# Optimization experiments

Hardware: AMD Instinct MI355X
Metric: run time of the kernel (lower is better)

## Reference

```python
import jax, jax.numpy as jnp
import numpy as np

DECAY = 0.99
EPSILON = 1e-05


def setup_inputs() -> dict:
    key = jax.random.key(0)
    k1, k2, k3, k4 = jax.random.split(key, 4)
    B, S, D, K = 16, 2048, 512, 2048
    x = jax.random.normal(k1, (B, S, D), dtype=jnp.float32)
    embed = jax.random.normal(k2, (K, D), dtype=jnp.float32)
    cluster_size = jax.random.uniform(k3, (K,), dtype=jnp.float32)
    embed_avg = jax.random.normal(k4, (K, D), dtype=jnp.float32)
    return {"x": x, "embed": embed, "cluster_size": cluster_size, "embed_avg": embed_avg}


def reference(x, embed, cluster_size, embed_avg):
    # x: [B,S,D]  embed: [K,D]  cluster_size: [K]  embed_avg: [K,D]
    B, S, D = x.shape
    K = embed.shape[0]
    xf = x.reshape(-1, D)  # [N,D], N=B*S

    # quantize(): negative squared euclidean distance, argmax over codebook
    x_sq = jnp.sum(xf * xf, axis=1, keepdims=True)            # [N,1]
    e_sq = jnp.sum(embed * embed, axis=1)[None, :]            # [1,K]
    dist = -(x_sq - 2.0 * (xf @ embed.T) + e_sq)              # [N,K]
    embed_ind = jnp.argmax(dist, axis=-1)                     # [N] int

    # dequantize
    quantize = embed[embed_ind].reshape(B, S, D)

    # training EMA updates (onehot.sum(0) and x^T @ onehot expressed as segment sums)
    ones = jnp.ones((xf.shape[0],), dtype=x.dtype)
    bins = jax.ops.segment_sum(ones, embed_ind, num_segments=K)        # [K] == onehot.sum(0)
    embed_sum_t = jax.ops.segment_sum(xf, embed_ind, num_segments=K)   # [K,D] == (x.T @ onehot).T

    new_cluster_size = cluster_size * DECAY + (1.0 - DECAY) * bins
    new_embed_avg = embed_avg * DECAY + (1.0 - DECAY) * embed_sum_t

    total = new_cluster_size.sum()
    smoothed = (new_cluster_size + EPSILON) / (total + K * EPSILON) * total  # laplace smoothing
    new_embed = new_embed_avg / smoothed[:, None]

    return (quantize,
            embed_ind.reshape(B, S),
            dist.reshape(B, S, K),
            new_cluster_size,
            new_embed_avg,
            new_embed)
```

## Files before the change

### kernel.cpp

```cpp
#include <hip/hip_runtime.h>

#define DECAY 0.99f
#define OMD   0.01f
#define EPS   1e-5f

constexpr int Bb = 16, Ss = 2048, Dd = 512, Kk = 2048;
constexpr int Nn = Bb * Ss;
constexpr int RP = 1088;

typedef __attribute__((ext_vector_type(8))) short short8;
typedef __attribute__((ext_vector_type(4))) float f32x4;

__device__ __forceinline__ unsigned short f2bf(float x) {
    unsigned u = __float_as_uint(x);
    unsigned r = (u + 0x7FFFu + ((u >> 16) & 1u)) >> 16;
    return (unsigned short)r;
}
__device__ __forceinline__ float bf2f(unsigned short u) {
    return __uint_as_float((unsigned)u << 16);
}

__device__ __forceinline__ void gload_lds16(const void* g, void* l) {
    __builtin_amdgcn_global_load_lds(
        (const __attribute__((address_space(1))) void*)g,
        (__attribute__((address_space(3))) void*)l, 16, 0, 0);
}

__device__ __forceinline__ short8 swap16(short8 v) {
    union { short8 s; unsigned u[4]; } a, b;
    a.s = v;
    #pragma unroll
    for (int i = 0; i < 4; ++i) b.u[i] = (a.u[i] >> 16) | (a.u[i] << 16);
    return b.s;
}

#define BARRIER() do { asm volatile("" ::: "memory"); \
                       __builtin_amdgcn_s_barrier();  \
                       asm volatile("" ::: "memory"); } while (0)

__global__ void rows_sq(const float* __restrict__ in, float* __restrict__ out, int nrows) {
    int row  = blockIdx.x * 4 + (threadIdx.x >> 6);
    int lane = threadIdx.x & 63;
    if (row >= nrows) return;
    const float4* p = (const float4*)(in + (size_t)row * Dd);
    float s = 0.f;
    #pragma unroll
    for (int i = 0; i < 2; ++i) {
        float4 v = p[lane + 64 * i];
        s += v.x * v.x + v.y * v.y + v.z * v.z + v.w * v.w;
    }
    #pragma unroll
    for (int off = 32; off; off >>= 1) s += __shfl_down(s, off);
    if (lane == 0) out[row] = s;
}

__global__ void conv_ilv(const float* __restrict__ in,
                         unsigned short* __restrict__ out,
                         float* __restrict__ sq) {
    int row  = blockIdx.x * 4 + (threadIdx.x >> 6);
    int lane = threadIdx.x & 63;
    const float4* p = (const float4*)(in + (size_t)row * Dd);
    uint4* o = (uint4*)(out + (size_t)row * RP);
    float s = 0.f;
    #pragma unroll
    for (int i = 0; i < 2; ++i) {
        int idx = lane + 64 * i;
        float4 v = p[idx];
        float f[4] = {v.x, v.y, v.z, v.w};
        unsigned d[4];
        #pragma unroll
        for (int j = 0; j < 4; ++j) {
            float x = f[j];
            s += x * x;
            unsigned short h = f2bf(x);
            unsigned short m = f2bf(x - bf2f(h));
            d[j] = ((unsigned)m << 16) | h;
        }
        o[idx] = make_uint4(d[0], d[1], d[2], d[3]);
    }
    #pragma unroll
    for (int off = 32; off; off >>= 1) s += __shfl_down(s, off);
    if (lane == 0) sq[row] = s;
}

__global__ __launch_bounds__(512, 1) void gemm_ilv(
    const unsigned short* __restrict__ xhm,
    const unsigned short* __restrict__ ehm,
    const float* __restrict__ xsq,
    const float* __restrict__ esq,
    float* __restrict__ dist,
    unsigned long long* __restrict__ packed)
{
    __shared__ unsigned short As[2][256][64];
    __shared__ unsigned short Bs[2][256][64];

    const int tid  = threadIdx.x;
    const int lane = tid & 63;
    const int wid  = tid >> 6;
    const int wr   = wid >> 2;
    const int wc   = wid & 3;

    int bid = blockIdx.x;
    int wg  = (bid & 7) * 128 + (bid >> 3);
    int mb  = wg >> 3, nb = wg & 7;
    const int row0 = mb * 256, col0 = nb * 256;

    f32x4 acc[8][4] = {};

    const int l8   = lane >> 3;
    const int csrc = (lane & 7) ^ l8;

    auto stageT = [&](const unsigned short* pl, unsigned short (*dst)[64],
                      int base, int t) {
        #pragma unroll
        for (int jj = 0; jj < 4; ++jj) {
            int rowbase = jj * 64 + wid * 8;
            int row = rowbase + l8;
            const unsigned short* src =
                pl + (size_t)(base + row) * RP + t * 64 + csrc * 8;
            gload_lds16(src, &dst[rowbase][0]);
        }
    };

    auto readA = [&](int d, int g, short8* out) {
        #pragma unroll
        for (int m = 0; m < 8; ++m) {
            int r = wr * 128 + m * 16 + (lane & 15);
            int c = (g * 4 + (lane >> 4)) ^ (r & 7);
            out[m] = *(const short8*)&As[d][r][c * 8];
        }
    };
    auto readB = [&](int d, int g, short8* out) {
        #pragma unroll
        for (int n = 0; n < 4; ++n) {
            int r = wc * 64 + n * 16 + (lane & 15);
            int c = (g * 4 + (lane >> 4)) ^ (r & 7);
            out[n] = *(const short8*)&Bs[d][r][c * 8];
        }
    };

    stageT(xhm, As[0], row0, 0);
    stageT(ehm, Bs[0], col0, 0);
    asm volatile("s_waitcnt vmcnt(0)" ::: "memory");
    BARRIER();

    for (int t = 0; t < 16; ++t) {
        const int cur = t & 1, nxt = cur ^ 1;
        if (t < 15) {
            stageT(xhm, As[nxt], row0, t + 1);
            stageT(ehm, Bs[nxt], col0, t + 1);
        }

        #pragma unroll
        for (int g = 0; g < 2; ++g) {
            short8 va[8], vb[4], vb2[4];
            readA(cur, g, va);
            readB(cur, g, vb);
            #pragma unroll
            for (int n = 0; n < 4; ++n) vb2[n] = swap16(vb[n]);
            #pragma unroll
            for (int m = 0; m < 8; ++m)
                #pragma unroll
                for (int n = 0; n < 4; ++n)
                    acc[m][n] = __builtin_amdgcn_mfma_f32_16x16x32_bf16(
                        va[m], vb[n], acc[m][n], 0, 0, 0);
            #pragma unroll
            for (int m = 0; m < 8; ++m)
                #pragma unroll
                for (int n = 0; n < 4; ++n)
                    acc[m][n] = __builtin_amdgcn_mfma_f32_16x16x32_bf16(
                        va[m], vb2[n], acc[m][n], 0, 0, 0);
        }

        asm volatile("s_waitcnt vmcnt(0)" ::: "memory");
        BARRIER();
    }

    const int jrow = (lane >> 4) * 4;
    const int ncol = lane & 15;
    #pragma unroll
    for (int m = 0; m < 8; ++m) {
        int rbase = row0 + wr * 128 + m * 16 + jrow;
        #pragma unroll
        for (int j = 0; j < 4; ++j) {
            int row = rbase + j;
            float xs = xsq[row];
            float best = -3.4e38f; int bi = 0;
            #pragma unroll
            for (int n = 0; n < 4; ++n) {
                int col = col0 + wc * 64 + n * 16 + ncol;
                float v = 2.f * acc[m][n][j] - xs - esq[col];
                dist[(size_t)row * Kk + col] = v;
                if (v > best) { best = v; bi = col; }
            }
            unsigned u = __float_as_uint(best);
            u = (u & 0x80000000u) ? ~u : (u | 0x80000000u);
            unsigned long long pk = ((unsigned long long)u << 32) | (unsigned)(~bi);
            #pragma unroll
            for (int off = 1; off < 16; off <<= 1) {
                unsigned long long o = __shfl_xor(pk, off);
                if (o > pk) pk = o;
            }
            if (ncol == 0) atomicMax(&packed[row], pk);
        }
    }
}

__global__ void gather_scatter_packed(const float* __restrict__ x,
                                      const float* __restrict__ embed,
                                      const unsigned long long* __restrict__ packed,
                                      float* __restrict__ quant,
                                      float* __restrict__ ind_f,
                                      float* __restrict__ esum,
                                      int* __restrict__ bins) {
    int n = blockIdx.x;
    int k = (int)(~(unsigned)(packed[n] & 0xFFFFFFFFull));
    int t = threadIdx.x;
    size_t xb = (size_t)n * Dd;
    size_t eb = (size_t)k * Dd;
    float v0 = x[xb + t];
    float v1 = x[xb + t + 256];
    quant[xb + t]       = embed[eb + t];
    quant[xb + t + 256] = embed[eb + t + 256];
    atomicAdd(&esum[eb + t],       v0);
    atomicAdd(&esum[eb + t + 256], v1);
    if (t == 0) { ind_f[n] = (float)k; atomicAdd(&bins[k], 1); }
}

#define BM 64
#define BN 64
#define BK 32
__global__ __launch_bounds__(256) void gemm_dist(
    const float* __restrict__ A, const float* __restrict__ Bm_,
    const float* __restrict__ xsq, const float* __restrict__ esq,
    float* __restrict__ dist)
{
    __shared__ float Asl[BK][BM + 4];
    __shared__ float Bsl[BK][BN + 4];
    int tid = threadIdx.x;
    int row0 = blockIdx.x * BM, col0 = blockIdx.y * BN;
    int tx = tid & 15, ty = tid >> 4;
    float acc[4][4] = {};
    int lr = tid >> 3, lc = (tid & 7) * 4;
    for (int d0 = 0; d0 < Dd; d0 += BK) {
        float4 a0 = *(const float4*)(A   + (size_t)(row0 + lr)      * Dd + d0 + lc);
        float4 a1 = *(const float4*)(A   + (size_t)(row0 + lr + 32) * Dd + d0 + lc);
        float4 b0 = *(const float4*)(Bm_ + (size_t)(col0 + lr)      * Dd + d0 + lc);
        float4 b1 = *(const float4*)(Bm_ + (size_t)(col0 + lr + 32) * Dd + d0 + lc);
        __syncthreads();
        Asl[lc + 0][lr] = a0.x; Asl[lc + 1][lr] = a0.y; Asl[lc + 2][lr] = a0.z; Asl[lc + 3][lr] = a0.w;
        Asl[lc + 0][lr + 32] = a1.x; Asl[lc + 1][lr + 32] = a1.y; Asl[lc + 2][lr + 32] = a1.z; Asl[lc + 3][lr + 32] = a1.w;
        Bsl[lc + 0][lr] = b0.x; Bsl[lc + 1][lr] = b0.y; Bsl[lc + 2][lr] = b0.z; Bsl[lc + 3][lr] = b0.w;
        Bsl[lc + 0][lr + 32] = b1.x; Bsl[lc + 1][lr + 32] = b1.y; Bsl[lc + 2][lr + 32] = b1.z; Bsl[lc + 3][lr + 32] = b1.w;
        __syncthreads();
        #pragma unroll
        for (int kd = 0; kd < BK; ++kd) {
            float4 av = *(const float4*)&Asl[kd][ty * 4];
            float4 bv = *(const float4*)&Bsl[kd][tx * 4];
            float a[4] = {av.x, av.y, av.z, av.w};
            float b[4] = {bv.x, bv.y, bv.z, bv.w};
            #pragma unroll
            for (int i = 0; i < 4; ++i)
                #pragma unroll
                for (int j = 0; j < 4; ++j)
                    acc[i][j] = fmaf(a[i], b[j], acc[i][j]);
        }
    }
    #pragma unroll
    for (int i = 0; i < 4; ++i) {
        int row = row0 + ty * 4 + i;
        float xs = xsq[row];
        float4 o;
        int col = col0 + tx * 4;
        o.x = 2.f * acc[i][0] - xs - esq[col + 0];
        o.y = 2.f * acc[i][1] - xs - esq[col + 1];
        o.z = 2.f * acc[i][2] - xs - esq[col + 2];
        o.w = 2.f * acc[i][3] - xs - esq[col + 3];
        *(float4*)(dist + (size_t)row * Kk + col) = o;
    }
}

__global__ void argmax_k(const float* __restrict__ dist,
                         float* __restrict__ ind_f, int* __restrict__ ind_i) {
    int row  = blockIdx.x * 4 + (threadIdx.x >> 6);
    int lane = threadIdx.x & 63;
    const float4* p = (const float4*)(dist + (size_t)row * Kk);
    float best = -3.4e38f;
    int bidx = 0;
    #pragma unroll
    for (int it = 0; it < Kk / 4 / 64; ++it) {
        int i = lane + it * 64;
        float4 v = p[i];
        int base = i * 4;
        if (v.x > best) { best = v.x; bidx = base + 0; }
        if (v.y > best) { best = v.y; bidx = base + 1; }
        if (v.z > best) { best = v.z; bidx = base + 2; }
        if (v.w > best) { best = v.w; bidx = base + 3; }
    }
    #pragma unroll
    for (int off = 32; off; off >>= 1) {
        float ov = __shfl_down(best, off);
        int   oi = __shfl_down(bidx, off);
        if (ov > best || (ov == best && oi < bidx)) { best = ov; bidx = oi; }
    }
    if (lane == 0) { ind_f[row] = (float)bidx; ind_i[row] = bidx; }
}

__global__ void gather_scatter(const float* __restrict__ x,
                               const float* __restrict__ embed,
                               const int* __restrict__ ind,
                               float* __restrict__ quant,
                               float* __restrict__ esum,
                               int* __restrict__ bins) {
    int n = blockIdx.x;
    int k = ind[n];
    int t = threadIdx.x;
    size_t xb = (size_t)n * Dd;
    size_t eb = (size_t)k * Dd;
    float v0 = x[xb + t];
    float v1 = x[xb + t + 256];
    quant[xb + t]       = embed[eb + t];
    quant[xb + t + 256] = embed[eb + t + 256];
    atomicAdd(&esum[eb + t],       v0);
    atomicAdd(&esum[eb + t + 256], v1);
    if (t == 0) atomicAdd(&bins[k], 1);
}

__global__ void finalize1(const float* __restrict__ cs, const int* __restrict__ bins,
                          float* __restrict__ ncs, float* __restrict__ total_ws) {
    __shared__ float red[16];
    int t = threadIdx.x;
    float s = 0.f;
    for (int k = t; k < Kk; k += 1024) {
        float v = cs[k] * DECAY + OMD * (float)bins[k];
        ncs[k] = v;
        s += v;
    }
    #pragma unroll
    for (int off = 32; off; off >>= 1) s += __shfl_down(s, off);
    if ((t & 63) == 0) red[t >> 6] = s;
    __syncthreads();
    if (t == 0) {
        float tot = 0.f;
        #pragma unroll
        for (int i = 0; i < 16; ++i) tot += red[i];
        total_ws[0] = tot;
    }
}

__global__ void finalize2(const float* __restrict__ ea, const float* __restrict__ esum,
                          const float* __restrict__ ncs, const float* __restrict__ total_ws,
                          float* __restrict__ nea, float* __restrict__ ne) {
    int idx = blockIdx.x * 256 + threadIdx.x;
    float total = total_ws[0];
    int k = idx >> 7;
    float sm = (ncs[k] + EPS) / (total + Kk * EPS) * total;
    float inv = 1.f / sm;
    float4 a = ((const float4*)ea)[idx];
    float4 s = ((const float4*)esum)[idx];
    float4 r;
    r.x = a.x * DECAY + OMD * s.x;
    r.y = a.y * DECAY + OMD * s.y;
    r.z = a.z * DECAY + OMD * s.z;
    r.w = a.w * DECAY + OMD * s.w;
    ((float4*)nea)[idx] = r;
    float4 e;
    e.x = r.x * inv; e.y = r.y * inv; e.z = r.z * inv; e.w = r.w * inv;
    ((float4*)ne)[idx] = e;
}

extern "C" void kernel_launch(void* const* d_in, const int* in_sizes, int n_in,
                              void* d_out, int out_size, void* d_ws, size_t ws_size,
                              hipStream_t stream) {
    const float* x     = (const float*)d_in[0];
    const float* embed = (const float*)d_in[1];
    const float* cs    = (const float*)d_in[2];
    const float* ea    = (const float*)d_in[3];

    float* out     = (float*)d_out;
    float* o_quant = out;
    float* o_ind   = o_quant + (size_t)Nn * Dd;
    float* o_dist  = o_ind + Nn;
    float* o_ncs   = o_dist + (size_t)Nn * Kk;
    float* o_nea   = o_ncs + Kk;
    float* o_ne    = o_nea + (size_t)Kk * Dd;

    size_t xp_elems = (size_t)3 * Nn * Dd;
    size_t ep_elems = (size_t)3 * Kk * Dd;
    char* w = (char*)d_ws;
    unsigned short* xp = (unsigned short*)w;                 w += xp_elems * 2;
    unsigned short* epp = (unsigned short*)w;                w += ep_elems * 2;
    float* xsq   = (float*)w;                                w += (size_t)Nn * 4;
    float* esq   = (float*)w;                                w += (size_t)Kk * 4;
    int*   ind_i = (int*)w;                                  w += (size_t)Nn * 4;
    int*   bins  = (int*)w;                                  w += (size_t)Kk * 4;
    float* esum  = (float*)w;                                w += (size_t)Kk * Dd * 4;
    unsigned long long* packed = (unsigned long long*)w;     w += (size_t)Nn * 8;
    float* total = (float*)w;                                w += 256;
    size_t need = (size_t)(w - (char*)d_ws);

    if (ws_size >= need) {
        hipMemsetAsync(bins, 0, (size_t)Kk * 4 + (size_t)Kk * Dd * 4 + (size_t)Nn * 8, stream);

        conv_ilv<<<Nn / 4, 256, 0, stream>>>(x, xp, xsq);
        conv_ilv<<<Kk / 4, 256, 0, stream>>>(embed, epp, esq);

        gemm_ilv<<<(Nn / 256) * (Kk / 256), 512, 0, stream>>>(
            xp, epp, xsq, esq, o_dist, packed);

        gather_scatter_packed<<<Nn, 256, 0, stream>>>(
            x, embed, packed, o_quant, o_ind, esum, bins);
    } else {
        float* fxsq  = (float*)d_ws;
        float* fesq  = fxsq + Nn;
        int*   find  = (int*)(fesq + Kk);
        int*   fbins = find + Nn;
        float* fesum = (float*)(fbins + Kk);
        float* ftot  = fesum + (size_t)Kk * Dd;
        xsq = fxsq; esq = fesq; ind_i = find; bins = fbins; esum = fesum; total = ftot;

        hipMemsetAsync(bins, 0, (size_t)(Kk + Kk * Dd) * sizeof(float), stream);
        rows_sq<<<Nn / 4, 256, 0, stream>>>(x, xsq, Nn);
        rows_sq<<<Kk / 4, 256, 0, stream>>>(embed, esq, Kk);
        dim3 g(Nn / BM, Kk / BN);
        gemm_dist<<<g, 256, 0, stream>>>(x, embed, xsq, esq, o_dist);
        argmax_k<<<Nn / 4, 256, 0, stream>>>(o_dist, o_ind, ind_i);
        gather_scatter<<<Nn, 256, 0, stream>>>(x, embed, ind_i, o_quant, esum, bins);
    }

    finalize1<<<1, 1024, 0, stream>>>(cs, bins, o_ncs, total);
    finalize2<<<(Kk * Dd / 4) / 256, 256, 0, stream>>>(ea, esum, o_ncs, total, o_nea, o_ne);
}
```

Measured before the change: 391.9 us.

## Switch distance GEMM to 32x32x16 MFMA tiles and vectorize gather-scatter

Replaces the 16x16x32 bf16 MFMA tiling with 32x32x16 MFMAs (4x2 accumulator tiles of 16 floats per wave). This lowers the LDS reads per flop and the MFMA instruction count, and raises the MFMA priority around the compute block. The epilogue is rewritten for the 32x32 output layout: esq is hoisted and the row-argmax reduction now spans 32 lanes. The gather/scatter kernel moves to float4 loads and stores with 128 threads per row. Costs include a different epilogue store pattern and higher accumulator register pressure.

```diff
diff --git a/kernel.cpp b/kernel.cpp
--- a/kernel.cpp
+++ b/kernel.cpp
@@ -10,6 +10,7 @@
 
 typedef __attribute__((ext_vector_type(8))) short short8;
 typedef __attribute__((ext_vector_type(4))) float f32x4;
+typedef __attribute__((ext_vector_type(16))) float f32x16;
 
 __device__ __forceinline__ unsigned short f2bf(float x) {
     unsigned u = __float_as_uint(x);
@@ -83,7 +84,7 @@
     if (lane == 0) sq[row] = s;
 }
 
-__global__ __launch_bounds__(512, 1) void gemm_ilv(
+__global__ __launch_bounds__(512, 1) void gemm_ilv32(
     const unsigned short* __restrict__ xhm,
     const unsigned short* __restrict__ ehm,
     const float* __restrict__ xsq,
@@ -105,7 +106,7 @@
     int mb  = wg >> 3, nb = wg & 7;
     const int row0 = mb * 256, col0 = nb * 256;
 
-    f32x4 acc[8][4] = {};
+    f32x16 acc[4][2] = {};
 
     const int l8   = lane >> 3;
     const int csrc = (lane & 7) ^ l8;
@@ -122,20 +123,20 @@
         }
     };
 
-    auto readA = [&](int d, int g, short8* out) {
-        #pragma unroll
-        for (int m = 0; m < 8; ++m) {
-            int r = wr * 128 + m * 16 + (lane & 15);
-            int c = (g * 4 + (lane >> 4)) ^ (r & 7);
-            out[m] = *(const short8*)&As[d][r][c * 8];
+    auto readA32 = [&](int d, int ks, short8* out) {
+        #pragma unroll
+        for (int mi = 0; mi < 4; ++mi) {
+            int r = wr * 128 + mi * 32 + (lane & 31);
+            int c = (ks * 2 + (lane >> 5)) ^ (r & 7);
+            out[mi] = *(const short8*)&As[d][r][c * 8];
         }
     };
-    auto readB = [&](int d, int g, short8* out) {
-        #pragma unroll
-        for (int n = 0; n < 4; ++n) {
-            int r = wc * 64 + n * 16 + (lane & 15);
-            int c = (g * 4 + (lane >> 4)) ^ (r & 7);
-            out[n] = *(const short8*)&Bs[d][r][c * 8];
+    auto readB32 = [&](int d, int ks, short8* out) {
+        #pragma unroll
+        for (int ni = 0; ni < 2; ++ni) {
+            int r = wc * 64 + ni * 32 + (lane & 31);
+            int c = (ks * 2 + (lane >> 5)) ^ (r & 7);
+            out[ni] = *(const short8*)&Bs[d][r][c * 8];
         }
     };
 
@@ -152,56 +153,58 @@
         }
 
         #pragma unroll
-        for (int g = 0; g < 2; ++g) {
-            short8 va[8], vb[4], vb2[4];
-            readA(cur, g, va);
-            readB(cur, g, vb);
+        for (int ks = 0; ks < 4; ++ks) {
+            short8 va[4], vb[2], vb2[2];
+            readA32(cur, ks, va);
+            readB32(cur, ks, vb);
+            vb2[0] = swap16(vb[0]); vb2[1] = swap16(vb[1]);
+            __builtin_amdgcn_s_setprio(1);
             #pragma unroll
-            for (int n = 0; n < 4; ++n) vb2[n] = swap16(vb[n]);
+            for (int mi = 0; mi < 4; ++mi)
+                #pragma unroll
+                for (int ni = 0; ni < 2; ++ni)
+                    acc[mi][ni] = __builtin_amdgcn_mfma_f32_32x32x16_bf16(
+                        va[mi], vb[ni], acc[mi][ni], 0, 0, 0);
             #pragma unroll
-            for (int m = 0; m < 8; ++m)
+            for (int mi = 0; mi < 4; ++mi)
                 #pragma unroll
-                for (int n = 0; n < 4; ++n)
-                    acc[m][n] = __builtin_amdgcn_mfma_f32_16x16x32_bf16(
-                        va[m], vb[n], acc[m][n], 0, 0, 0);
-            #pragma unroll
-            for (int m = 0; m < 8; ++m)
-                #pragma unroll
-                for (int n = 0; n < 4; ++n)
-                    acc[m][n] = __builtin_amdgcn_mfma_f32_16x16x32_bf16(
-                        va[m], vb2[n], acc[m][n], 0, 0, 0);
+                for (int ni = 0; ni < 2; ++ni)
+                    acc[mi][ni] = __builtin_amdgcn_mfma_f32_32x32x16_bf16(
+                        va[mi], vb2[ni], acc[mi][ni], 0, 0, 0);
+            __builtin_amdgcn_s_setprio(0);
         }
 
         asm volatile("s_waitcnt vmcnt(0)" ::: "memory");
         BARRIER();
     }
 
-    const int jrow = (lane >> 4) * 4;
-    const int ncol = lane & 15;
-    #pragma unroll
-    for (int m = 0; m < 8; ++m) {
-        int rbase = row0 + wr * 128 + m * 16 + jrow;
-        #pragma unroll
-        for (int j = 0; j < 4; ++j) {
-            int row = rbase + j;
+    const int lcol = lane & 31;
+    const int lhalf = lane >> 5;
+    float esq0[2];
+    esq0[0] = esq[col0 + wc * 64 + lcol];
+    esq0[1] = esq[col0 + wc * 64 + 32 + lcol];
+    #pragma unroll
+    for (int mi = 0; mi < 4; ++mi) {
+        #pragma unroll
+        for (int reg = 0; reg < 16; ++reg) {
+            int row = row0 + wr * 128 + mi * 32 + (reg & 3) + 8 * (reg >> 2) + 4 * lhalf;
             float xs = xsq[row];
-            float best = -3.4e38f; int bi = 0;
-            #pragma unroll
-            for (int n = 0; n < 4; ++n) {
-                int col = col0 + wc * 64 + n * 16 + ncol;
-                float v = 2.f * acc[m][n][j] - xs - esq[col];
-                dist[(size_t)row * Kk + col] = v;
-                if (v > best) { best = v; bi = col; }
-            }
+            float v0 = 2.f * acc[mi][0][reg] - xs - esq0[0];
+            float v1 = 2.f * acc[mi][1][reg] - xs - esq0[1];
+            int c0 = col0 + wc * 64 + lcol;
+            dist[(size_t)row * Kk + c0]      = v0;
+            dist[(size_t)row * Kk + c0 + 32] = v1;
+            float best = v0; int bi = c0;
+            if (v1 > best) { best = v1; bi = c0 + 32; }
             unsigned u = __float_as_uint(best);
             u = (u & 0x80000000u) ? ~u : (u | 0x80000000u);
             unsigned long long pk = ((unsigned long long)u << 32) | (unsigned)(~bi);
             #pragma unroll
-            for (int off = 1; off < 16; off <<= 1) {
+            for (int off = 1; off < 32; off <<= 1) {
                 unsigned long long o = __shfl_xor(pk, off);
                 if (o > pk) pk = o;
             }
-            if (ncol == 0) atomicMax(&packed[row], pk);
+            if (lcol == 0) atomicMax(&packed[row], pk);
         }
     }
 }
@@ -216,14 +219,16 @@
     int n = blockIdx.x;
     int k = (int)(~(unsigned)(packed[n] & 0xFFFFFFFFull));
     int t = threadIdx.x;
-    size_t xb = (size_t)n * Dd;
-    size_t eb = (size_t)k * Dd;
-    float v0 = x[xb + t];
-    float v1 = x[xb + t + 256];
-    quant[xb + t]       = embed[eb + t];
-    quant[xb + t + 256] = embed[eb + t + 256];
-    atomicAdd(&esum[eb + t],       v0);
-    atomicAdd(&esum[eb + t + 256], v1);
+    const float4* xv = (const float4*)(x + (size_t)n * Dd);
+    const float4* ev = (const float4*)(embed + (size_t)k * Dd);
+    float4* qv = (float4*)(quant + (size_t)n * Dd);
+    float4 vx = xv[t];
+    qv[t] = ev[t];
+    float* ep = esum + (size_t)k * Dd + t * 4;
+    atomicAdd(&ep[0], vx.x);
+    atomicAdd(&ep[1], vx.y);
+    atomicAdd(&ep[2], vx.z);
+    atomicAdd(&ep[3], vx.w);
     if (t == 0) { ind_f[n] = (float)k; atomicAdd(&bins[k], 1); }
 }
 
@@ -405,10 +410,10 @@
         conv_ilv<<<Nn / 4, 256, 0, stream>>>(x, xp, xsq);
         conv_ilv<<<Kk / 4, 256, 0, stream>>>(embed, epp, esq);
 
-        gemm_ilv<<<(Nn / 256) * (Kk / 256), 512, 0, stream>>>(
+        gemm_ilv32<<<(Nn / 256) * (Kk / 256), 512, 0, stream>>>(
             xp, epp, xsq, esq, o_dist, packed);
 
-        gather_scatter_packed<<<Nn, 256, 0, stream>>>(
+        gather_scatter_packed<<<Nn, 128, 0, stream>>>(
             x, embed, packed, o_quant, o_ind, esum, bins);
     } else {
         float* fxsq  = (float*)d_ws;
```

After: 686.9 us. 1.75x slower.
